# Kernel tuning notes

Measured on AMD Instinct MI355X. Metric: run time of the kernel, lower is better.

Reference implementation:

```python
import jax, jax.numpy as jnp
import numpy as np

B, H, T, S, D, V = 4, 16, 512, 512, 1024, 32000
EPS = 1e-12


def setup_inputs() -> dict:
    key = jax.random.key(0)
    ks = jax.random.split(key, 12)
    return {
        "decoder_attention": jax.random.uniform(ks[0], (B, H, T, S), dtype=jnp.float32),
        "decoder_last_hidden_state": jax.random.normal(ks[1], (B, T, D), dtype=jnp.float32),
        "enc_input_ids": jax.random.randint(ks[2], (B, S), 0, V, dtype=jnp.int64),
        "logits": jax.random.normal(ks[3], (B, T, V), dtype=jnp.float32),
        "decoder_input_embeds": jax.random.normal(ks[4], (B, T, D), dtype=jnp.float32),
        "encoder_last_hidden_state": jax.random.normal(ks[5], (B, S, D), dtype=jnp.float32),
        # Linear(d_model, 1) params (weight as [D] vector, scalar bias)
        "w_logits": jax.random.normal(ks[6], (D,), dtype=jnp.float32) / np.sqrt(D),
        "b_logits": jnp.zeros((), dtype=jnp.float32),
        "w_embeds": jax.random.normal(ks[7], (D,), dtype=jnp.float32) / np.sqrt(D),
        "b_embeds": jnp.zeros((), dtype=jnp.float32),
        "w_enc": jax.random.normal(ks[8], (D,), dtype=jnp.float32) / np.sqrt(D),
        "b_enc": jnp.zeros((), dtype=jnp.float32),
        "bias": jnp.zeros((), dtype=jnp.float32),
    }


def reference(decoder_attention, decoder_last_hidden_state, enc_input_ids, logits,
              decoder_input_embeds, encoder_last_hidden_state,
              w_logits, b_logits, w_embeds, b_embeds, w_enc, b_enc, bias):
    g_distribution = jax.nn.softmax(logits, axis=-1)                      # [B,T,V]
    c_attention = jnp.mean(decoder_attention, axis=1)                      # [B,T,S]

    # scatter_add attention into vocab space: c_dist[b,t,enc_ids[b,s]] += c_attn[b,t,s]
    b_idx = jnp.arange(B)[:, None, None]
    t_idx = jnp.arange(T)[None, :, None]
    v_idx = enc_input_ids[:, None, :]                                      # [B,1,S]
    c_distribution = jnp.zeros_like(g_distribution).at[b_idx, t_idx, v_idx].add(c_attention)

    ctx = jnp.einsum('bts,bsd->btd', c_attention, encoder_last_hidden_state)  # [B,T,D]
    gate_logit = (decoder_last_hidden_state @ w_logits + b_logits
                  + decoder_input_embeds @ w_embeds + b_embeds
                  + ctx @ w_enc + b_enc + bias)                             # [B,T]
    p_copy = jax.nn.sigmoid(gate_logit)[..., None]                          # [B,T,1]

    mixed = p_copy * c_distribution + (1.0 - p_copy) * g_distribution
    return jnp.log(mixed + EPS)
```

## Files before the change

### kernel.cpp

```cpp
#include <hip/hip_runtime.h>
#include <math.h>

constexpr int NB = 4;
constexpr int NH = 16;
constexpr int NT = 512;
constexpr int NS = 512;
constexpr int ND = 1024;
constexpr int NV = 32000;
constexpr int NV4 = NV / 4;
constexpr float EPS = 1e-12f;

constexpr int HSIZE = 2048;
constexpr int BLK = 1024;

__global__ void eproj_kernel(const float* __restrict__ E, const float* __restrict__ w_enc,
                             float* __restrict__ e_proj) {
    int gid = blockIdx.x * blockDim.x + threadIdx.x;
    int w = gid >> 6;
    int lane = gid & 63;
    if (w >= NB * NS) return;
    const float4* e4 = (const float4*)(E + (size_t)w * ND);
    const float4* w4 = (const float4*)w_enc;
    float acc = 0.f;
#pragma unroll
    for (int i = lane; i < ND / 4; i += 64) {
        float4 a = e4[i], b = w4[i];
        acc += a.x * b.x + a.y * b.y + a.z * b.z + a.w * b.w;
    }
    for (int off = 32; off > 0; off >>= 1) acc += __shfl_down(acc, off, 64);
    if (lane == 0) e_proj[w] = acc;
}

__device__ __forceinline__ float esum4(float4 v) {
    return __expf(v.x) + __expf(v.y) + __expf(v.z) + __expf(v.w);
}

__global__ __launch_bounds__(1024, 8) void out_kernel(
    const float* __restrict__ A,
    const float* __restrict__ logits,
    const int*   __restrict__ ids,
    const float* __restrict__ dlhs,
    const float* __restrict__ die,
    const float* __restrict__ e_proj,
    const float* __restrict__ w_logits, const float* __restrict__ w_embeds,
    const float* __restrict__ b_logits, const float* __restrict__ b_embeds,
    const float* __restrict__ b_enc, const float* __restrict__ bias,
    float* __restrict__ out) {
    __shared__ int   hkey[HSIZE];
    __shared__ float hval[HSIZE];
    __shared__ float sred[36];

    const int row = blockIdx.x;
    const int tid = threadIdx.x;
    const int b = row / NT;
    const int t = row % NT;

    for (int i = tid; i < HSIZE; i += BLK) {
        hkey[i] = -1;
        hval[i] = 0.f;
    }

    float cmean = 0.f;
    if (tid < NS) {
        const float* Ap = A + ((size_t)b * NH * NT + t) * NS + tid;
        float acc = 0.f;
#pragma unroll
        for (int h = 0; h < NH; ++h) acc += Ap[(size_t)h * NT * NS];
        cmean = acc * (1.0f / NH);
    }
    __syncthreads();

    float gsum = 0.f;
    if (tid < ND / 4) {
        const float4* x1 = (const float4*)(dlhs + (size_t)row * ND);
        const float4* w1 = (const float4*)w_logits;
        const float4* x2 = (const float4*)(die + (size_t)row * ND);
        const float4* w2 = (const float4*)w_embeds;
        float4 a0 = x1[tid], b0 = w1[tid];
        gsum += a0.x * b0.x + a0.y * b0.y + a0.z * b0.z + a0.w * b0.w;
        float4 a1 = x2[tid], b1 = w2[tid];
        gsum += a1.x * b1.x + a1.y * b1.y + a1.z * b1.z + a1.w * b1.w;
    }
    if (tid < NS) {
        gsum += cmean * e_proj[(size_t)b * NS + tid];
        int id = ids[b * NS + tid];
        unsigned h = ((unsigned)id * 2654435761u) >> 21;
        for (int probe = 0; probe < HSIZE; ++probe) {
            int prev = atomicCAS(&hkey[h], -1, id);
            if (prev == -1 || prev == id) {
                atomicAdd(&hval[h], cmean);
                break;
            }
            h = (h + 1) & (HSIZE - 1);
        }
    }

    const float4* L4 = (const float4*)(logits + (size_t)row * NV);
    const bool has7 = (tid + 7168 < NV4);
    float4 r0 = L4[tid];
    float4 r1 = L4[tid + 1024];
    float4 r2 = L4[tid + 2048];
    float4 r3 = L4[tid + 3072];
    float4 r4 = L4[tid + 4096];
    float4 r5 = L4[tid + 5120];
    float4 r6 = L4[tid + 6144];
    float4 r7;
    float zsum = esum4(r0) + esum4(r1) + esum4(r2) + esum4(r3)
               + esum4(r4) + esum4(r5) + esum4(r6);
    if (has7) {
        r7 = L4[tid + 7168];
        zsum += esum4(r7);
    }

    for (int off = 32; off > 0; off >>= 1) {
        zsum += __shfl_down(zsum, off, 64);
        gsum += __shfl_down(gsum, off, 64);
    }
    const int wave = tid >> 6;
    const int lane = tid & 63;
    if (lane == 0) { sred[wave] = zsum; sred[16 + wave] = gsum; }
    __syncthreads();
    if (tid == 0) {
        float Z = 0.f, G = 0.f;
#pragma unroll
        for (int i = 0; i < 16; ++i) { Z += sred[i]; G += sred[16 + i]; }
        G += b_logits[0] + b_embeds[0] + b_enc[0] + bias[0];
        float p = 1.f / (1.f + __expf(-G));
        float a = (1.f - p) / Z;
        sred[32] = a;
        sred[33] = p;
        sred[34] = __logf(a);
    }
    __syncthreads();
    const float a  = sred[32];
    const float p  = sred[33];
    const float la = sred[34];

    float4* O4 = (float4*)(out + (size_t)row * NV);
#define XFRM(v) { float tx;                                                \
        tx = v.x + la; v.x = (tx > -20.f) ? tx : __logf(__expf(tx) + EPS); \
        tx = v.y + la; v.y = (tx > -20.f) ? tx : __logf(__expf(tx) + EPS); \
        tx = v.z + la; v.z = (tx > -20.f) ? tx : __logf(__expf(tx) + EPS); \
        tx = v.w + la; v.w = (tx > -20.f) ? tx : __logf(__expf(tx) + EPS); }
    XFRM(r0); O4[tid]        = r0;
    XFRM(r1); O4[tid + 1024] = r1;
    XFRM(r2); O4[tid + 2048] = r2;
    XFRM(r3); O4[tid + 3072] = r3;
    XFRM(r4); O4[tid + 4096] = r4;
    XFRM(r5); O4[tid + 5120] = r5;
    XFRM(r6); O4[tid + 6144] = r6;
    if (has7) {
        XFRM(r7); O4[tid + 7168] = r7;
    }
#undef XFRM
    __syncthreads();

    for (int i = tid; i < HSIZE; i += BLK) {
        int id = hkey[i];
        if (id >= 0) {
            float x = logits[(size_t)row * NV + id];
            out[(size_t)row * NV + id] = __logf(a * __expf(x) + p * hval[i] + EPS);
        }
    }
}

extern "C" void kernel_launch(void* const* d_in, const int* in_sizes, int n_in,
                              void* d_out, int out_size, void* d_ws, size_t ws_size,
                              hipStream_t stream) {
    const float* dec_attn = (const float*)d_in[0];
    const float* dlhs     = (const float*)d_in[1];
    const int*   ids      = (const int*)d_in[2];
    const float* logits   = (const float*)d_in[3];
    const float* die      = (const float*)d_in[4];
    const float* enc      = (const float*)d_in[5];
    const float* w_logits = (const float*)d_in[6];
    const float* b_logits = (const float*)d_in[7];
    const float* w_embeds = (const float*)d_in[8];
    const float* b_embeds = (const float*)d_in[9];
    const float* w_enc    = (const float*)d_in[10];
    const float* b_enc    = (const float*)d_in[11];
    const float* bias     = (const float*)d_in[12];
    float* out = (float*)d_out;

    float* e_proj = (float*)d_ws;

    {
        int waves = NB * NS;
        eproj_kernel<<<(waves * 64) / 256, 256, 0, stream>>>(enc, w_enc, e_proj);
    }
    {
        out_kernel<<<NB * NT, BLK, 0, stream>>>(
            dec_attn, logits, ids, dlhs, die, e_proj,
            w_logits, w_embeds, b_logits, b_embeds, b_enc, bias, out);
    }
}
```

Measured before the change: 530.0 us.

## Halve block size, re-read logits in second pass, stagger small work per block

The output kernel now runs 512-thread blocks. Instead of holding the whole logits row in registers across the reduction, it streams the row twice: once for the exp-sum and again for the transform and store. Odd and even blocks do the gate/hash work before or after the streaming pass, so their memory phases are staggered. Per-wave partials are combined with shared-memory atomics and each thread computes the gate scalars itself, which removes one barrier. This lowers register pressure and lets more blocks fit per CU, at the cost of reading logits twice, relying on cache to absorb the second read.

Measured after the change: 552.5 us. 4.2% more time.

```diff
diff --git a/kernel.cpp b/kernel.cpp
--- a/kernel.cpp
+++ b/kernel.cpp
@@ -11,7 +11,7 @@
 constexpr float EPS = 1e-12f;
 
 constexpr int HSIZE = 2048;
-constexpr int BLK = 1024;
+constexpr int BLK = 512;
 
 __global__ void eproj_kernel(const float* __restrict__ E, const float* __restrict__ w_enc,
                              float* __restrict__ e_proj) {
@@ -35,7 +35,7 @@
     return __expf(v.x) + __expf(v.y) + __expf(v.z) + __expf(v.w);
 }
 
-__global__ __launch_bounds__(1024, 8) void out_kernel(
+__global__ __launch_bounds__(512, 8) void out_kernel(
     const float* __restrict__ A,
     const float* __restrict__ logits,
     const int*   __restrict__ ids,
@@ -48,7 +48,7 @@
     float* __restrict__ out) {
     __shared__ int   hkey[HSIZE];
     __shared__ float hval[HSIZE];
-    __shared__ float sred[36];
+    __shared__ float sZ, sG;
 
     const int row = blockIdx.x;
     const int tid = threadIdx.x;
@@ -59,30 +59,30 @@
         hkey[i] = -1;
         hval[i] = 0.f;
     }
-
-    float cmean = 0.f;
-    if (tid < NS) {
-        const float* Ap = A + ((size_t)b * NH * NT + t) * NS + tid;
-        float acc = 0.f;
+    if (tid == 0) { sZ = 0.f; sG = 0.f; }
+
+    const float* Ap = A + ((size_t)b * NH * NT + t) * NS + tid;
+    float cacc = 0.f;
 #pragma unroll
-        for (int h = 0; h < NH; ++h) acc += Ap[(size_t)h * NT * NS];
-        cmean = acc * (1.0f / NH);
-    }
+    for (int h = 0; h < NH; ++h) cacc += Ap[(size_t)h * NT * NS];
+    const float cmean = cacc * (1.0f / NH);
     __syncthreads();
 
-    float gsum = 0.f;
-    if (tid < ND / 4) {
-        const float4* x1 = (const float4*)(dlhs + (size_t)row * ND);
-        const float4* w1 = (const float4*)w_logits;
-        const float4* x2 = (const float4*)(die + (size_t)row * ND);
-        const float4* w2 = (const float4*)w_embeds;
-        float4 a0 = x1[tid], b0 = w1[tid];
-        gsum += a0.x * b0.x + a0.y * b0.y + a0.z * b0.z + a0.w * b0.w;
-        float4 a1 = x2[tid], b1 = w2[tid];
-        gsum += a1.x * b1.x + a1.y * b1.y + a1.z * b1.z + a1.w * b1.w;
-    }
-    if (tid < NS) {
-        gsum += cmean * e_proj[(size_t)b * NS + tid];
+    float zsum = 0.f, gsum = 0.f;
+    const float4* L4 = (const float4*)(logits + (size_t)row * NV);
+
+    auto do_small = [&]() {
+        if (tid < ND / 4) {
+            const float4* x1 = (const float4*)(dlhs + (size_t)row * ND);
+            const float4* w1 = (const float4*)w_logits;
+            const float4* x2 = (const float4*)(die + (size_t)row * ND);
+            const float4* w2 = (const float4*)w_embeds;
+            float4 a0 = x1[tid], b0 = w1[tid];
+            gsum += a0.x * b0.x + a0.y * b0.y + a0.z * b0.z + a0.w * b0.w;
+            float4 a1 = x2[tid], b1 = w2[tid];
+            gsum += a1.x * b1.x + a1.y * b1.y + a1.z * b1.z + a1.w * b1.w;
+        }
+        gsum += cmean * e_proj[b * NS + tid];
         int id = ids[b * NS + tid];
         unsigned h = ((unsigned)id * 2654435761u) >> 21;
         for (int probe = 0; probe < HSIZE; ++probe) {
@@ -93,48 +93,55 @@
             }
             h = (h + 1) & (HSIZE - 1);
         }
-    }
-
-    const float4* L4 = (const float4*)(logits + (size_t)row * NV);
-    const bool has7 = (tid + 7168 < NV4);
-    float4 r0 = L4[tid];
-    float4 r1 = L4[tid + 1024];
-    float4 r2 = L4[tid + 2048];
-    float4 r3 = L4[tid + 3072];
-    float4 r4 = L4[tid + 4096];
-    float4 r5 = L4[tid + 5120];
-    float4 r6 = L4[tid + 6144];
-    float4 r7;
-    float zsum = esum4(r0) + esum4(r1) + esum4(r2) + esum4(r3)
-               + esum4(r4) + esum4(r5) + esum4(r6);
-    if (has7) {
-        r7 = L4[tid + 7168];
-        zsum += esum4(r7);
-    }
+    };
+
+    auto do_stream = [&]() {
+        {
+            float4 v0 = L4[tid];
+            float4 v1 = L4[tid + 512];
+            float4 v2 = L4[tid + 1024];
+            float4 v3 = L4[tid + 1536];
+            float4 v4 = L4[tid + 2048];
+            zsum += esum4(v0) + esum4(v1) + esum4(v2) + esum4(v3) + esum4(v4);
+        }
+        {
+            float4 v0 = L4[tid + 2560];
+            float4 v1 = L4[tid + 3072];
+            float4 v2 = L4[tid + 3584];
+            float4 v3 = L4[tid + 4096];
+            float4 v4 = L4[tid + 4608];
+            zsum += esum4(v0) + esum4(v1) + esum4(v2) + esum4(v3) + esum4(v4);
+        }
+        {
+            float4 v0 = L4[tid + 5120];
+            float4 v1 = L4[tid + 5632];
+            float4 v2 = L4[tid + 6144];
+            float4 v3 = L4[tid + 6656];
+            float4 v4 = L4[tid + 7168];
+            zsum += esum4(v0) + esum4(v1) + esum4(v2) + esum4(v3) + esum4(v4);
+        }
+        if (tid < NV4 - 7680) {
+            zsum += esum4(L4[tid + 7680]);
+        }
+    };
+
+    if (blockIdx.x & 1) { do_small(); do_stream(); }
+    else                { do_stream(); do_small(); }
 
     for (int off = 32; off > 0; off >>= 1) {
         zsum += __shfl_down(zsum, off, 64);
         gsum += __shfl_down(gsum, off, 64);
     }
-    const int wave = tid >> 6;
-    const int lane = tid & 63;
-    if (lane == 0) { sred[wave] = zsum; sred[16 + wave] = gsum; }
+    if ((tid & 63) == 0) {
+        atomicAdd(&sZ, zsum);
+        atomicAdd(&sG, gsum);
+    }
     __syncthreads();
-    if (tid == 0) {
-        float Z = 0.f, G = 0.f;
-#pragma unroll
-        for (int i = 0; i < 16; ++i) { Z += sred[i]; G += sred[16 + i]; }
-        G += b_logits[0] + b_embeds[0] + b_enc[0] + bias[0];
-        float p = 1.f / (1.f + __expf(-G));
-        float a = (1.f - p) / Z;
-        sred[32] = a;
-        sred[33] = p;
-        sred[34] = __logf(a);
-    }
-    __syncthreads();
-    const float a  = sred[32];
-    const float p  = sred[33];
-    const float la = sred[34];
+
+    const float G  = sG + b_logits[0] + b_embeds[0] + b_enc[0] + bias[0];
+    const float p  = 1.f / (1.f + __expf(-G));
+    const float a  = (1.f - p) / sZ;
+    const float la = __logf(a);
 
     float4* O4 = (float4*)(out + (size_t)row * NV);
 #define XFRM(v) { float tx;                                                \
@@ -142,15 +149,45 @@
         tx = v.y + la; v.y = (tx > -20.f) ? tx : __logf(__expf(tx) + EPS); \
         tx = v.z + la; v.z = (tx > -20.f) ? tx : __logf(__expf(tx) + EPS); \
         tx = v.w + la; v.w = (tx > -20.f) ? tx : __logf(__expf(tx) + EPS); }
-    XFRM(r0); O4[tid]        = r0;
-    XFRM(r1); O4[tid + 1024] = r1;
-    XFRM(r2); O4[tid + 2048] = r2;
-    XFRM(r3); O4[tid + 3072] = r3;
-    XFRM(r4); O4[tid + 4096] = r4;
-    XFRM(r5); O4[tid + 5120] = r5;
-    XFRM(r6); O4[tid + 6144] = r6;
-    if (has7) {
-        XFRM(r7); O4[tid + 7168] = r7;
+    {
+        float4 v0 = L4[tid];
+        float4 v1 = L4[tid + 512];
+        float4 v2 = L4[tid + 1024];
+        float4 v3 = L4[tid + 1536];
+        float4 v4 = L4[tid + 2048];
+        XFRM(v0); O4[tid]        = v0;
+        XFRM(v1); O4[tid + 512]  = v1;
+        XFRM(v2); O4[tid + 1024] = v2;
+        XFRM(v3); O4[tid + 1536] = v3;
+        XFRM(v4); O4[tid + 2048] = v4;
+    }
+    {
+        float4 v0 = L4[tid + 2560];
+        float4 v1 = L4[tid + 3072];
+        float4 v2 = L4[tid + 3584];
+        float4 v3 = L4[tid + 4096];
+        float4 v4 = L4[tid + 4608];
+        XFRM(v0); O4[tid + 2560] = v0;
+        XFRM(v1); O4[tid + 3072] = v1;
+        XFRM(v2); O4[tid + 3584] = v2;
+        XFRM(v3); O4[tid + 4096] = v3;
+        XFRM(v4); O4[tid + 4608] = v4;
+    }
+    {
+        float4 v0 = L4[tid + 5120];
+        float4 v1 = L4[tid + 5632];
+        float4 v2 = L4[tid + 6144];
+        float4 v3 = L4[tid + 6656];
+        float4 v4 = L4[tid + 7168];
+        XFRM(v0); O4[tid + 5120] = v0;
+        XFRM(v1); O4[tid + 5632] = v1;
+        XFRM(v2); O4[tid + 6144] = v2;
+        XFRM(v3); O4[tid + 6656] = v3;
+        XFRM(v4); O4[tid + 7168] = v4;
+    }
+    if (tid < NV4 - 7680) {
+        float4 v = L4[tid + 7680];
+        XFRM(v); O4[tid + 7680] = v;
     }
 #undef XFRM
     __syncthreads();
```
